# Kernel optimization log

Measured on AMD Instinct MI355X. Metric: run time of the kernel, lower is better.

## Reference

```python
import jax, jax.numpy as jnp
import numpy as np

N = 50000          # nodes
E = 1600000        # edges (avg degree 32)
DIMS = [128, 128, 128, 64]  # in_features + hidden_dims


def setup_inputs() -> dict:
    key = jax.random.key(0)
    ks = jax.random.split(key, 10)
    x = jax.random.normal(ks[0], (N, DIMS[0]), dtype=jnp.float32)
    edge_index = jax.random.randint(ks[1], (2, E), 0, N, dtype=jnp.int64)
    edge_weight = jax.random.uniform(ks[2], (E,), dtype=jnp.float32)
    params = {}
    for i in range(3):
        fan_in, fan_out = DIMS[i], DIMS[i + 1]
        scale = jnp.sqrt(6.0 / (fan_in + fan_out))  # glorot as in PyG GCNConv lin
        params[f"W{i+1}"] = jax.random.uniform(ks[3 + i], (fan_in, fan_out), jnp.float32, -scale, scale)
        params[f"b{i+1}"] = jnp.zeros((fan_out,), jnp.float32)
    return dict(x=x, edge_index=edge_index, edge_weight=edge_weight, **params)


def gcn_norm(edge_index, edge_weight, n):
    # PyG gcn_norm: add self-loops (weight 1), symmetric deg^-1/2 normalization
    src, dst = edge_index[0], edge_index[1]
    loop = jnp.arange(n, dtype=src.dtype)
    src = jnp.concatenate([src, loop])
    dst = jnp.concatenate([dst, loop])
    ew = jnp.concatenate([edge_weight, jnp.ones((n,), edge_weight.dtype)])
    deg = jax.ops.segment_sum(ew, dst, num_segments=n)  # degree at target
    dinv = jnp.where(deg > 0, jax.lax.rsqrt(jnp.maximum(deg, 1e-30)), 0.0)
    return src, dst, dinv[src] * ew * dinv[dst]


def gcn_conv(x, W, b, src, dst, norm, n):
    h = x @ W                                   # [N, out]
    msg = h[src] * norm[:, None]                # gather + edge scale
    agg = jax.ops.segment_sum(msg, dst, num_segments=n)  # scatter-add to targets
    return agg + b


def reference(x, edge_index, edge_weight, W1, b1, W2, b2, W3, b3):
    n = x.shape[0]
    src, dst, norm = gcn_norm(edge_index, edge_weight, n)
    x = jax.nn.relu(gcn_conv(x, W1, b1, src, dst, norm, n))
    x = jax.nn.relu(gcn_conv(x, W2, b2, src, dst, norm, n))
    return gcn_conv(x, W3, b3, src, dst, norm, n)
```

## Files before the change

kernel.cpp:

```cpp
#include <hip/hip_runtime.h>
#include <hip/hip_bf16.h>
#include <hip/hip_fp16.h>


#define K_IN 128
#define FIX_SCALE 8388608.0f
#define CE 4096

typedef _Float16 f16x8 __attribute__((ext_vector_type(8)));
typedef float f32x4 __attribute__((ext_vector_type(4)));

__global__ __launch_bounds__(1024) void part_count_wt(
    const int* __restrict__ dst, int* __restrict__ counts,
    unsigned short* __restrict__ lrank, int nb, int nblk, int e,
    const float* __restrict__ W1, const float* __restrict__ W2,
    const float* __restrict__ W3, _Float16* __restrict__ Wt1,
    _Float16* __restrict__ Wt2, _Float16* __restrict__ Wt3) {
    int blk = blockIdx.x;
    if (blk >= nblk) {
        int i = (blk - nblk) * 1024 + threadIdx.x;
        if (i < 128 * 128) {
            int k = i >> 7, nn = i & 127;
            Wt1[(size_t)nn * 128 + k] = (_Float16)W1[i];
        } else if (i < 2 * 128 * 128) {
            int j = i - 128 * 128, k = j >> 7, nn = j & 127;
            Wt2[(size_t)nn * 128 + k] = (_Float16)W2[j];
        } else if (i < 2 * 128 * 128 + 64 * 128) {
            int l = i - 2 * 128 * 128, k = l >> 6, nn = l & 63;
            Wt3[(size_t)nn * 128 + k] = (_Float16)W3[l];
        }
        return;
    }
    __shared__ int c[256];
    int t = threadIdx.x;
    for (int i = t; i < nb; i += 1024) c[i] = 0;
    __syncthreads();
    int b0 = blk * CE;
#pragma unroll
    for (int j = 0; j < 4; j++) {
        int i = b0 + j * 1024 + t;
        if (i < e) {
            int b = dst[i] >> 8;
            int r = atomicAdd(&c[b], 1);
            lrank[i] = (unsigned short)r;
        }
    }
    __syncthreads();
    for (int i = t; i < nb; i += 1024) counts[(size_t)i * nblk + blk] = c[i];
}

__global__ __launch_bounds__(256) void reduce_kernel(const int* __restrict__ v,
                                                     int* __restrict__ bs, int m) {
    __shared__ int s[256];
    int t = threadIdx.x, i = blockIdx.x * 256 + t;
    s[t] = (i < m) ? v[i] : 0;
    __syncthreads();
    for (int off = 128; off > 0; off >>= 1) {
        if (t < off) s[t] += s[t + off];
        __syncthreads();
    }
    if (t == 0) bs[blockIdx.x] = s[0];
}

__global__ __launch_bounds__(1024) void scanb1024(const int* __restrict__ bs,
                                                  int* __restrict__ bo, int nbb) {
    __shared__ int s[1024];
    int t = threadIdx.x;
    s[t] = (t < nbb) ? bs[t] : 0;
    __syncthreads();
    for (int off = 1; off < 1024; off <<= 1) {
        int cur = s[t];
        int add = (t >= off) ? s[t - off] : 0;
        __syncthreads();
        s[t] = cur + add;
        __syncthreads();
    }
    if (t < nbb) bo[t] = (t == 0) ? 0 : s[t - 1];
}

__global__ __launch_bounds__(256) void scanw_kernel(const int* __restrict__ v,
                                                    const int* __restrict__ bo,
                                                    int* __restrict__ outp, int m) {
    __shared__ int s[256];
    int t = threadIdx.x, i = blockIdx.x * 256 + t;
    int c = (i < m) ? v[i] : 0;
    s[t] = c;
    __syncthreads();
    for (int off = 1; off < 256; off <<= 1) {
        int cur = s[t];
        int add = (t >= off) ? s[t - off] : 0;
        __syncthreads();
        s[t] = cur + add;
        __syncthreads();
    }
    if (i < m) outp[i] = bo[blockIdx.x] + (s[t] - c);
}

__global__ __launch_bounds__(1024) void part_scatter(const int* __restrict__ src,
                                                     const int* __restrict__ dst,
                                                     const float* __restrict__ ew,
                                                     const int* __restrict__ base,
                                                     const unsigned short* __restrict__ lrank,
                                                     int2* __restrict__ arr1,
                                                     int nblk, int e) {
    int t = threadIdx.x, blk = blockIdx.x;
    int b0 = blk * CE;
#pragma unroll
    for (int j = 0; j < 4; j++) {
        int i = b0 + j * 1024 + t;
        if (i < e) {
            int d = dst[i];
            int b = d >> 8;
            int pos = base[(size_t)b * nblk + blk] + lrank[i];
            arr1[pos] = make_int2((src[i] << 8) | (d & 255), __float_as_int(ew[i]));
        }
    }
}

__global__ __launch_bounds__(1024) void bucket_csr(const int2* __restrict__ arr1,
                                                   const int* __restrict__ base,
                                                   unsigned short* __restrict__ rank2,
                                                   float* __restrict__ dinv,
                                                   int* __restrict__ row_ptr,
                                                   int2* __restrict__ ep,
                                                   int nb, int nblk, int n, int e) {
    __shared__ unsigned long long pk[256];
    __shared__ int nbase[256];
    __shared__ float ldsdinv[256];
    __shared__ int ss[256];
    int t = threadIdx.x, b = blockIdx.x;
    int beg = base[(size_t)b * nblk];
    int end = (b + 1 < nb) ? base[(size_t)(b + 1) * nblk] : e;
    if (t < 256) pk[t] = 0ULL;
    __syncthreads();
    for (int i = beg + t; i < end; i += 1024) {
        int2 a = arr1[i];
        int ld = a.x & 255;
        float w = __int_as_float(a.y);
        unsigned long long fx = (unsigned long long)(unsigned int)(w * FIX_SCALE + 0.5f);
        unsigned long long old = atomicAdd(&pk[ld], (fx << 32) | 1ULL);
        rank2[i] = (unsigned short)(old & 0xffffffffULL);
    }
    __syncthreads();
    int cnt = (t < 256) ? (int)(pk[t] & 0xffffffffULL) : 0;
    if (t < 256) ss[t] = cnt;
    __syncthreads();
    for (int off = 1; off < 256; off <<= 1) {
        int cur = 0, add = 0;
        if (t < 256) { cur = ss[t]; add = (t >= off) ? ss[t - off] : 0; }
        __syncthreads();
        if (t < 256) ss[t] = cur + add;
        __syncthreads();
    }
    if (t < 256) {
        nbase[t] = ss[t] - cnt;
        int d = b * 256 + t;
        if (d < n) {
            float dv = rsqrtf(1.0f + (float)(unsigned int)(pk[t] >> 32) * (1.0f / FIX_SCALE));
            dinv[d] = dv;
            ldsdinv[t] = dv;
            row_ptr[d] = beg + nbase[t];
        }
    }
    __syncthreads();
    for (int i = beg + t; i < end; i += 1024) {
        int2 a = arr1[i];
        int ld = a.x & 255;
        int pos = beg + nbase[ld] + rank2[i];
        float w = __int_as_float(a.y) * ldsdinv[ld];
        ep[pos] = make_int2(a.x >> 8, __float_as_int(w));
    }
}

template <int NOUT, bool XF16, bool FUSEVAL>
__global__ __launch_bounds__(256) void mfma_gemm(const void* __restrict__ Xv,
                                                 const _Float16* __restrict__ Wt,
                                                 _Float16* __restrict__ H, int n,
                                                 int gGemm, int vblk,
                                                 int2* __restrict__ ep,
                                                 const float* __restrict__ dinv,
                                                 int* __restrict__ row_ptr, int e) {
    constexpr int CTW = NOUT / 64;
    __shared__ _Float16 Xs[64][136];
    __shared__ _Float16 Ws[NOUT][136];
    int t = threadIdx.x;
    if (FUSEVAL && (int)blockIdx.x >= gGemm) {
        int vb = blockIdx.x - gGemm;
        if (vb == 0 && t == 0) row_ptr[n] = e;
        for (int i = vb * 256 + t; i < e; i += vblk * 256) {
            int2 a = ep[i];
            float w = __int_as_float(a.y) * dinv[a.x];
            ep[i] = make_int2(a.x << 8, __float_as_int(w));
        }
        return;
    }
    int row0 = blockIdx.x * 64;

    for (int i = t * 8; i < NOUT * K_IN; i += 2048) {
        int nn = i >> 7, k = i & 127;
        *(uint4*)&Ws[nn][k] = *(const uint4*)&Wt[i];
    }
    if (XF16) {
        const _Float16* X = (const _Float16*)Xv;
        for (int i = t * 8; i < 64 * K_IN; i += 2048) {
            int r = i >> 7, k = i & 127;
            int row = row0 + r;
            uint4 v = make_uint4(0u, 0u, 0u, 0u);
            if (row < n) v = *(const uint4*)(X + (size_t)row * K_IN + k);
            *(uint4*)&Xs[r][k] = v;
        }
    } else {
        const float* X = (const float*)Xv;
        for (int i = t * 4; i < 64 * K_IN; i += 1024) {
            int r = i >> 7, k = i & 127;
            int row = row0 + r;
            float4 x4 = make_float4(0.f, 0.f, 0.f, 0.f);
            if (row < n) x4 = *(const float4*)(X + (size_t)row * K_IN + k);
            union { _Float16 h[4]; uint2 u; } uu;
            uu.h[0] = (_Float16)x4.x; uu.h[1] = (_Float16)x4.y;
            uu.h[2] = (_Float16)x4.z; uu.h[3] = (_Float16)x4.w;
            *(uint2*)&Xs[r][k] = uu.u;
        }
    }
    __syncthreads();

    int lane = t & 63, w = t >> 6;
    int m = lane & 15, g = lane >> 4;
    f32x4 acc[4][CTW];
#pragma unroll
    for (int mt = 0; mt < 4; mt++)
#pragma unroll
        for (int ct = 0; ct < CTW; ct++) acc[mt][ct] = (f32x4){0.f, 0.f, 0.f, 0.f};

#pragma unroll
    for (int kt = 0; kt < 4; kt++) {
        int kb = kt * 32 + g * 8;
        f16x8 a[4];
#pragma unroll
        for (int mt = 0; mt < 4; mt++) a[mt] = *(const f16x8*)&Xs[mt * 16 + m][kb];
#pragma unroll
        for (int ct = 0; ct < CTW; ct++) {
            int nn = w * (16 * CTW) + ct * 16 + m;
            f16x8 b = *(const f16x8*)&Ws[nn][kb];
#pragma unroll
            for (int mt = 0; mt < 4; mt++)
                acc[mt][ct] = __builtin_amdgcn_mfma_f32_16x16x32_f16(a[mt], b, acc[mt][ct], 0, 0, 0);
        }
    }

#pragma unroll
    for (int mt = 0; mt < 4; mt++) {
#pragma unroll
        for (int r = 0; r < 4; r++) {
            int row = row0 + mt * 16 + g * 4 + r;
            if (row < n) {
#pragma unroll
                for (int ct = 0; ct < CTW; ct++)
                    H[(size_t)row * NOUT + w * (16 * CTW) + ct * 16 + m] =
                        (_Float16)acc[mt][ct][r];
            }
        }
    }
}

template <int F, bool RELU, bool OF16>
__global__ __launch_bounds__(256) void agg_kernel(const __half* __restrict__ H,
                                                  const int* __restrict__ row_ptr,
                                                  const int2* __restrict__ ep,
                                                  const float* __restrict__ dinv,
                                                  const float* __restrict__ bias,
                                                  void* __restrict__ outv, int n) {
    constexpr int LPE = (F == 128) ? 16 : 8;
    constexpr int EPW = 64 / LPE;
    constexpr int UNC = (F == 128) ? 4 : 2;
    int wid = threadIdx.x >> 6;
    int lane = threadIdx.x & 63;
    int node = blockIdx.x * 4 + wid;
    if (node >= n) return;

    int start = __builtin_amdgcn_readfirstlane(row_ptr[node]);
    int end   = __builtin_amdgcn_readfirstlane(row_ptr[node + 1]);
    float di = dinv[node];
    float sw = di * di;

    int g  = lane / LPE;
    int fl = lane & (LPE - 1);
    const unsigned flb = (unsigned)fl * 16u;
    const char* Hb = (const char*)H;

    float acc[8];
    {
        uint4 sv = *(const uint4*)(Hb + (size_t)node * (F * 2) + flb);
        const __half2* sh = (const __half2*)&sv;
        float gm = (g == 0) ? sw : 0.0f;
#pragma unroll
        for (int j = 0; j < 4; j++) {
            float2 f = __half22float2(sh[j]);
            acc[2 * j]     = gm * f.x;
            acc[2 * j + 1] = gm * f.y;
        }
    }

    int len = end - start;
    int nch = (len + EPW - 1) / EPW;
    int pg  = start + g;

    auto ldep = [&](int c) -> int2 {
        int p = pg + c * EPW;
        int q = (p < end) ? p : (end - 1);
        int2 t = ep[q];
        if (p >= end) t.y = 0;
        return t;
    };

    if (nch > 0) {
        int2 e[UNC];
#pragma unroll
        for (int u = 0; u < UNC; u++) e[u] = ldep(u);
        for (int c0 = 0; c0 < nch; c0 += UNC) {
            uint4 v[UNC];
#pragma unroll
            for (int u = 0; u < UNC; u++) {
                unsigned off = (unsigned)e[u].x;
                if (F == 64) off >>= 1;
                v[u] = *(const uint4*)(Hb + (off + flb));
            }
            int2 e2[UNC];
#pragma unroll
            for (int u = 0; u < UNC; u++) e2[u] = ldep(c0 + UNC + u);
#pragma unroll
            for (int u = 0; u < UNC; u++) {
                float w = __int_as_float(e[u].y);
                const __half2* h2 = (const __half2*)&v[u];
#pragma unroll
                for (int j = 0; j < 4; j++) {
                    float2 f = __half22float2(h2[j]);
                    acc[2 * j]     = fmaf(w, f.x, acc[2 * j]);
                    acc[2 * j + 1] = fmaf(w, f.y, acc[2 * j + 1]);
                }
            }
#pragma unroll
            for (int u = 0; u < UNC; u++) e[u] = e2[u];
        }
    }

#pragma unroll
    for (int mask = LPE; mask < 64; mask <<= 1) {
#pragma unroll
        for (int j = 0; j < 8; j++) acc[j] += __shfl_xor(acc[j], mask, 64);
    }

    if (g == 0) {
        float4 b0 = *(const float4*)(bias + fl * 8);
        float4 b1 = *(const float4*)(bias + fl * 8 + 4);
        float o[8] = {acc[0] + b0.x, acc[1] + b0.y, acc[2] + b0.z, acc[3] + b0.w,
                      acc[4] + b1.x, acc[5] + b1.y, acc[6] + b1.z, acc[7] + b1.w};
        if (RELU) {
#pragma unroll
            for (int j = 0; j < 8; j++) o[j] = fmaxf(o[j], 0.0f);
        }
        if (OF16) {
            union { __half2 h[4]; uint4 u; } r;
#pragma unroll
            for (int j = 0; j < 4; j++) r.h[j] = __floats2half2_rn(o[2 * j], o[2 * j + 1]);
            *(uint4*)((char*)outv + (size_t)node * (F * 2) + flb) = r.u;
        } else {
            float* op = (float*)outv + (size_t)node * F + fl * 8;
            *(float4*)op       = make_float4(o[0], o[1], o[2], o[3]);
            *(float4*)(op + 4) = make_float4(o[4], o[5], o[6], o[7]);
        }
    }
}


extern "C" void kernel_launch(void* const* d_in, const int* in_sizes, int n_in,
                              void* d_out, int out_size, void* d_ws, size_t ws_size,
                              hipStream_t stream) {
    const float* x   = (const float*)d_in[0];
    const int*   ei  = (const int*)d_in[1];
    const float* ew  = (const float*)d_in[2];
    const float* W1  = (const float*)d_in[3];
    const float* b1  = (const float*)d_in[4];
    const float* W2  = (const float*)d_in[5];
    const float* b2  = (const float*)d_in[6];
    const float* W3  = (const float*)d_in[7];
    const float* b3  = (const float*)d_in[8];
    float* out = (float*)d_out;

    const int N = in_sizes[0] / K_IN;
    const int E = in_sizes[2];
    const int* src = ei;
    const int* dst = ei + E;

    const int NB   = (N + 255) >> 8;
    const int NBLK = (E + CE - 1) / CE;
    const int M    = NB * NBLK;
    const int NBB  = (M + 255) / 256;
    const int NWT  = (2 * 128 * 128 + 64 * 128 + 1023) / 1024;
    const int VBLK = 1024;

    char* w = (char*)d_ws;
    auto alloc = [&](size_t bytes) {
        void* p = (void*)w;
        w += (bytes + 255) & ~(size_t)255;
        return p;
    };
    int*            counts = (int*)alloc((size_t)M * 4);
    int*            base   = (int*)alloc((size_t)M * 4);
    int*            bsM    = (int*)alloc((size_t)NBB * 4);
    int*            boM    = (int*)alloc((size_t)NBB * 4);
    unsigned short* lrank  = (unsigned short*)alloc((size_t)E * 2);
    int2*           arr1   = (int2*)alloc((size_t)E * 8);
    float*          dinv   = (float*)alloc((size_t)N * 4);
    int*            row_ptr= (int*)alloc((size_t)(N + 1) * 4);
    int2*           ep     = (int2*)alloc((size_t)E * 8);
    _Float16*       Wt1    = (_Float16*)alloc(128 * 128 * 2);
    _Float16*       Wt2    = (_Float16*)alloc(128 * 128 * 2);
    _Float16*       Wt3    = (_Float16*)alloc(64 * 128 * 2);
    _Float16*       bufH   = (_Float16*)alloc((size_t)N * 128 * 2);
    _Float16*       bufX   = (_Float16*)alloc((size_t)N * 128 * 2);

    int gGemm = (N + 63) / 64;
    int gAgg  = (N + 3) / 4;

    part_count_wt<<<NBLK + NWT, 1024, 0, stream>>>(dst, counts, lrank, NB, NBLK, E,
                                                   W1, W2, W3, Wt1, Wt2, Wt3);
    reduce_kernel<<<NBB, 256, 0, stream>>>(counts, bsM, M);
    scanb1024<<<1, 1024, 0, stream>>>(bsM, boM, NBB);
    scanw_kernel<<<NBB, 256, 0, stream>>>(counts, boM, base, M);
    part_scatter<<<NBLK, 1024, 0, stream>>>(src, dst, ew, base, lrank, arr1, NBLK, E);
    bucket_csr<<<NB, 1024, 0, stream>>>(arr1, base, lrank, dinv, row_ptr, ep,
                                        NB, NBLK, N, E);

    mfma_gemm<128, false, true><<<gGemm + VBLK, 256, 0, stream>>>(
        x, Wt1, bufH, N, gGemm, VBLK, ep, dinv, row_ptr, E);
    agg_kernel<128, true, true><<<gAgg, 256, 0, stream>>>((const __half*)bufH, row_ptr, ep,
                                                          dinv, b1, bufX, N);
    mfma_gemm<128, true, false><<<gGemm, 256, 0, stream>>>(
        bufX, Wt2, bufH, N, gGemm, 0, nullptr, nullptr, nullptr, 0);
    agg_kernel<128, true, true><<<gAgg, 256, 0, stream>>>((const __half*)bufH, row_ptr, ep,
                                                          dinv, b2, bufX, N);
    mfma_gemm<64, true, false><<<gGemm, 256, 0, stream>>>(
        bufX, Wt3, bufH, N, gGemm, 0, nullptr, nullptr, nullptr, 0);
    agg_kernel<64, false, false><<<gAgg, 256, 0, stream>>>((const __half*)bufH, row_ptr, ep,
                                                           dinv, b3, out, N);
}
```

Before: 311.6 us.

## Split aggregation feature columns across blocks with 8-byte gathers per lane

The aggregation kernel now splits each node's feature row into 64-byte column chunks, each handled by a separate block, with 8 lanes per edge loading 8 bytes each and 8 edges processed per wavefront batch. The grid grows by the chunk count (4 for 128 features, 2 for 64). Edge-list loads and fp16 output stores become nontemporal, and the software prefetch of the next edge batch is dropped. This raises parallelism and may give more cache-friendly column access, but each edge record is now read once per chunk and each gather is narrower.

```diff
diff --git a/kernel.cpp b/kernel.cpp
--- a/kernel.cpp
+++ b/kernel.cpp
@@ -270,12 +270,12 @@
                                                   const float* __restrict__ dinv,
                                                   const float* __restrict__ bias,
                                                   void* __restrict__ outv, int n) {
-    constexpr int LPE = (F == 128) ? 16 : 8;
-    constexpr int EPW = 64 / LPE;
-    constexpr int UNC = (F == 128) ? 4 : 2;
+    constexpr int NCH = (F * 2) / 64;
+    constexpr int UNC = 4;
     int wid = threadIdx.x >> 6;
     int lane = threadIdx.x & 63;
-    int node = blockIdx.x * 4 + wid;
+    int chunk = blockIdx.x & (NCH - 1);
+    int node = (blockIdx.x / NCH) * 4 + wid;
     if (node >= n) return;
 
     int start = __builtin_amdgcn_readfirstlane(row_ptr[node]);
@@ -283,91 +283,88 @@
     float di = dinv[node];
     float sw = di * di;
 
-    int g  = lane / LPE;
-    int fl = lane & (LPE - 1);
-    const unsigned flb = (unsigned)fl * 16u;
+    int es = lane >> 3;
+    int fl = lane & 7;
+    const unsigned cb = (unsigned)chunk * 64u + (unsigned)fl * 8u;
     const char* Hb = (const char*)H;
 
-    float acc[8];
+    float acc[4];
     {
-        uint4 sv = *(const uint4*)(Hb + (size_t)node * (F * 2) + flb);
+        uint2 sv = *(const uint2*)(Hb + (size_t)node * (F * 2) + cb);
         const __half2* sh = (const __half2*)&sv;
-        float gm = (g == 0) ? sw : 0.0f;
-#pragma unroll
-        for (int j = 0; j < 4; j++) {
-            float2 f = __half22float2(sh[j]);
-            acc[2 * j]     = gm * f.x;
-            acc[2 * j + 1] = gm * f.y;
-        }
+        float gm = (es == 0) ? sw : 0.0f;
+        float2 f0 = __half22float2(sh[0]), f1 = __half22float2(sh[1]);
+        acc[0] = gm * f0.x; acc[1] = gm * f0.y;
+        acc[2] = gm * f1.x; acc[3] = gm * f1.y;
     }
 
     int len = end - start;
-    int nch = (len + EPW - 1) / EPW;
-    int pg  = start + g;
-
-    auto ldep = [&](int c) -> int2 {
-        int p = pg + c * EPW;
-        int q = (p < end) ? p : (end - 1);
-        int2 t = ep[q];
-        if (p >= end) t.y = 0;
-        return t;
-    };
-
-    if (nch > 0) {
-        int2 e[UNC];
-#pragma unroll
-        for (int u = 0; u < UNC; u++) e[u] = ldep(u);
-        for (int c0 = 0; c0 < nch; c0 += UNC) {
-            uint4 v[UNC];
+    if (len > 0) {
+        int nbat = (len + 7) >> 3;
+        for (int c0 = 0; c0 < nbat; c0 += UNC) {
+            int nb = nbat - c0;
+            if (nb > UNC) nb = UNC;
+            int2 e[UNC];
+            uint2 v[UNC];
 #pragma unroll
             for (int u = 0; u < UNC; u++) {
-                unsigned off = (unsigned)e[u].x;
-                if (F == 64) off >>= 1;
-                v[u] = *(const uint4*)(Hb + (off + flb));
-            }
-            int2 e2[UNC];
-#pragma unroll
-            for (int u = 0; u < UNC; u++) e2[u] = ldep(c0 + UNC + u);
-#pragma unroll
-            for (int u = 0; u < UNC; u++) {
-                float w = __int_as_float(e[u].y);
-                const __half2* h2 = (const __half2*)&v[u];
-#pragma unroll
-                for (int j = 0; j < 4; j++) {
-                    float2 f = __half22float2(h2[j]);
-                    acc[2 * j]     = fmaf(w, f.x, acc[2 * j]);
-                    acc[2 * j + 1] = fmaf(w, f.y, acc[2 * j + 1]);
+                if (u < nb) {
+                    int p = start + (c0 + u) * 8 + es;
+                    int q = (p < end) ? p : end - 1;
+                    long long raw = __builtin_nontemporal_load((const long long*)&ep[q]);
+                    int2 t;
+                    t.x = (int)(unsigned)(raw & 0xffffffffLL);
+                    t.y = (int)(raw >> 32);
+                    if (p >= end) t.y = 0;
+                    e[u] = t;
                 }
             }
 #pragma unroll
-            for (int u = 0; u < UNC; u++) e[u] = e2[u];
-        }
-    }
-
-#pragma unroll
-    for (int mask = LPE; mask < 64; mask <<= 1) {
-#pragma unroll
-        for (int j = 0; j < 8; j++) acc[j] += __shfl_xor(acc[j], mask, 64);
-    }
-
-    if (g == 0) {
-        float4 b0 = *(const float4*)(bias + fl * 8);
-        float4 b1 = *(const float4*)(bias + fl * 8 + 4);
-        float o[8] = {acc[0] + b0.x, acc[1] + b0.y, acc[2] + b0.z, acc[3] + b0.w,
-                      acc[4] + b1.x, acc[5] + b1.y, acc[6] + b1.z, acc[7] + b1.w};
+            for (int u = 0; u < UNC; u++) {
+                if (u < nb) {
+                    unsigned off = (unsigned)e[u].x;
+                    if (F == 64) off >>= 1;
+                    v[u] = *(const uint2*)(Hb + (off + cb));
+                }
+            }
+#pragma unroll
+            for (int u = 0; u < UNC; u++) {
+                if (u < nb) {
+                    float w = __int_as_float(e[u].y);
+                    const __half2* h2 = (const __half2*)&v[u];
+                    float2 f0 = __half22float2(h2[0]), f1 = __half22float2(h2[1]);
+                    acc[0] = fmaf(w, f0.x, acc[0]);
+                    acc[1] = fmaf(w, f0.y, acc[1]);
+                    acc[2] = fmaf(w, f1.x, acc[2]);
+                    acc[3] = fmaf(w, f1.y, acc[3]);
+                }
+            }
+        }
+    }
+
+#pragma unroll
+    for (int mask = 8; mask < 64; mask <<= 1) {
+#pragma unroll
+        for (int j = 0; j < 4; j++) acc[j] += __shfl_xor(acc[j], mask, 64);
+    }
+
+    if (es == 0) {
+        float4 b4 = *(const float4*)(bias + chunk * 32 + fl * 4);
+        float o0 = acc[0] + b4.x, o1 = acc[1] + b4.y;
+        float o2 = acc[2] + b4.z, o3 = acc[3] + b4.w;
         if (RELU) {
-#pragma unroll
-            for (int j = 0; j < 8; j++) o[j] = fmaxf(o[j], 0.0f);
+            o0 = fmaxf(o0, 0.f); o1 = fmaxf(o1, 0.f);
+            o2 = fmaxf(o2, 0.f); o3 = fmaxf(o3, 0.f);
         }
         if (OF16) {
-            union { __half2 h[4]; uint4 u; } r;
-#pragma unroll
-            for (int j = 0; j < 4; j++) r.h[j] = __floats2half2_rn(o[2 * j], o[2 * j + 1]);
-            *(uint4*)((char*)outv + (size_t)node * (F * 2) + flb) = r.u;
+            union { __half2 h[2]; long long ll; } r;
+            r.h[0] = __floats2half2_rn(o0, o1);
+            r.h[1] = __floats2half2_rn(o2, o3);
+            __builtin_nontemporal_store(
+                r.ll, (long long*)((char*)outv + (size_t)node * (F * 2) + cb));
         } else {
-            float* op = (float*)outv + (size_t)node * F + fl * 8;
-            *(float4*)op       = make_float4(o[0], o[1], o[2], o[3]);
-            *(float4*)(op + 4) = make_float4(o[4], o[5], o[6], o[7]);
+            *(float4*)((float*)outv + (size_t)node * F + chunk * 32 + fl * 4) =
+                make_float4(o0, o1, o2, o3);
         }
     }
 }
@@ -434,14 +431,14 @@
 
     mfma_gemm<128, false, true><<<gGemm + VBLK, 256, 0, stream>>>(
         x, Wt1, bufH, N, gGemm, VBLK, ep, dinv, row_ptr, E);
-    agg_kernel<128, true, true><<<gAgg, 256, 0, stream>>>((const __half*)bufH, row_ptr, ep,
-                                                          dinv, b1, bufX, N);
+    agg_kernel<128, true, true><<<gAgg * 4, 256, 0, stream>>>((const __half*)bufH, row_ptr, ep,
+                                                              dinv, b1, bufX, N);
     mfma_gemm<128, true, false><<<gGemm, 256, 0, stream>>>(
         bufX, Wt2, bufH, N, gGemm, 0, nullptr, nullptr, nullptr, 0);
-    agg_kernel<128, true, true><<<gAgg, 256, 0, stream>>>((const __half*)bufH, row_ptr, ep,
-                                                          dinv, b2, bufX, N);
+    agg_kernel<128, true, true><<<gAgg * 4, 256, 0, stream>>>((const __half*)bufH, row_ptr, ep,
+                                                              dinv, b2, bufX, N);
     mfma_gemm<64, true, false><<<gGemm, 256, 0, stream>>>(
         bufX, Wt3, bufH, N, gGemm, 0, nullptr, nullptr, nullptr, 0);
-    agg_kernel<64, false, false><<<gAgg, 256, 0, stream>>>((const __half*)bufH, row_ptr, ep,
-                                                           dinv, b3, out, N);
-}
+    agg_kernel<64, false, false><<<gAgg * 2, 256, 0, stream>>>((const __half*)bufH, row_ptr, ep,
+                                                               dinv, b3, out, N);
+}
```

Result: slower. 521.1 us (+67.2%).
